# Kernel tuning notes

Hardware: AMD Instinct MI355X
Metric: run time of the kernel (lower is better)

The kernel has to match this reference:

```python
import jax, jax.numpy as jnp
import numpy as np

E = 8        # num_experts
TOPK = 2     # num_experts_per_tok
D = 1024     # n_embd
H = 2816     # grok FFN hidden dim (multiple_of-rounded 2/3*4*D)
B, T = 4, 2048
COEFF = 0.01 # moe_aux_loss_coeff


def setup_inputs() -> dict:
    key = jax.random.key(0)
    ks = jax.random.split(key, 8)
    s = 0.02  # weight scale so activations stay well-conditioned
    return {
        "x": jax.random.normal(ks[0], (B, T, D), jnp.float32),
        "gate_w": jax.random.normal(ks[1], (D, E), jnp.float32) * s,
        "expert_gate": jax.random.normal(ks[2], (E, D, H), jnp.float32) * s,
        "expert_up": jax.random.normal(ks[3], (E, D, H), jnp.float32) * s,
        "expert_down": jax.random.normal(ks[4], (E, H, D), jnp.float32) * s,
        "shared_gate": jax.random.normal(ks[5], (D, H), jnp.float32) * s,
        "shared_up": jax.random.normal(ks[6], (D, H), jnp.float32) * s,
        "shared_down": jax.random.normal(ks[7], (H, D), jnp.float32) * s,
    }


def _grok_ffn(x, g, u, d):
    # down(gelu(gate(x)) * up(x)); torch F.gelu default = exact erf gelu
    return (jax.nn.gelu(x @ g, approximate=False) * (x @ u)) @ d


def reference(x, gate_w, expert_gate, expert_up, expert_down,
              shared_gate, shared_up, shared_down):
    Bb, Tt, Dd = x.shape
    N = Bb * Tt
    xf = x.reshape(N, Dd)

    # --- router ---
    logits = (xf @ gate_w).astype(jnp.float32)            # (N, E)
    top_logits, top_idx = jax.lax.top_k(logits, TOPK)     # (N, K)
    top_w = jax.nn.softmax(top_logits, axis=-1)           # (N, K)
    gates = jax.nn.softmax(logits, axis=-1)               # (N, E)
    f = jnp.mean(jax.nn.one_hot(top_idx[:, 0], E, dtype=jnp.float32), axis=0)
    P = gates.mean(axis=0)
    aux_loss = COEFF * E * jnp.sum(f * P)

    # dense combine weights (N, E): 0 for unassigned experts
    comb = jnp.zeros((N, E), xf.dtype).at[
        jnp.arange(N)[:, None], top_idx].add(top_w.astype(xf.dtype))

    # --- experts: loop over small fixed E, weight-masked dense FFN ---
    out = jnp.zeros_like(xf)
    for e in range(E):
        ye = _grok_ffn(xf, expert_gate[e], expert_up[e], expert_down[e])
        out = out + comb[:, e:e + 1] * ye

    out = out.reshape(Bb, Tt, Dd)
    out = out + _grok_ffn(xf, shared_gate, shared_up, shared_down).reshape(Bb, Tt, Dd)
    return out, aux_loss
```

## Files before the change

kernel.cpp:

```cpp
#include <hip/hip_runtime.h>
#include <hip/hip_bf16.h>

#define NTOK 8192
#define DIM  1024
#define HID  2816
#define ROWS_CAP 25600
#define TCAP 200

typedef __bf16 bf16x8 __attribute__((ext_vector_type(8)));
typedef float  f32x4  __attribute__((ext_vector_type(4)));

__device__ __forceinline__ unsigned short f2bf(float f) {
  unsigned int x = __float_as_uint(f);
  unsigned int r = (x + 0x7fffu + ((x >> 16) & 1u)) >> 16;
  return (unsigned short)r;
}
__device__ __forceinline__ float gelu_erf(float g) {
  return 0.5f * g * (1.0f + erff(g * 0.70710678118654752f));
}

__device__ __forceinline__ void gload16(const void* g, void* l) {
  __builtin_amdgcn_global_load_lds(
      (__attribute__((address_space(1))) void*)(g),
      (__attribute__((address_space(3))) void*)(l), 16, 0, 0);
}

__device__ __forceinline__ void pipe_barrier() {
  asm volatile("s_waitcnt vmcnt(0)" ::: "memory");
  __builtin_amdgcn_s_barrier();
  __builtin_amdgcn_sched_barrier(0);
}


__global__ __launch_bounds__(256) void k_cast_bf16(const float4* __restrict__ in,
                                                   ushort4* __restrict__ out, int n4) {
  int i = blockIdx.x * 256 + threadIdx.x;
  if (i >= n4) return;
  float4 v = in[i];
  out[i] = make_ushort4(f2bf(v.x), f2bf(v.y), f2bf(v.z), f2bf(v.w));
}

__global__ __launch_bounds__(256) void k_transpose_bf16(const float* __restrict__ in,
                                                        unsigned short* __restrict__ out,
                                                        int R, int C) {
  __shared__ float t[32][33];
  size_t base = (size_t)blockIdx.z * R * C;
  in += base; out += base;
  int c0 = blockIdx.x * 32, r0 = blockIdx.y * 32;
  int tx = threadIdx.x, ty = threadIdx.y;
  #pragma unroll
  for (int i = ty; i < 32; i += 8)
    t[i][tx] = in[(size_t)(r0 + i) * C + c0 + tx];
  __syncthreads();
  #pragma unroll
  for (int i = ty; i < 32; i += 8)
    out[(size_t)(c0 + i) * R + r0 + tx] = f2bf(t[tx][i]);
}


__global__ __launch_bounds__(256) void k_router(const float* __restrict__ x,
                                                const float* __restrict__ gw,
                                                int* __restrict__ top_idx,
                                                float* __restrict__ top_w,
                                                int* __restrict__ counts,
                                                float* __restrict__ f_cnt,
                                                float* __restrict__ P_sum) {
  __shared__ float s_p[8];
  __shared__ int   s_cnt[8];
  __shared__ int   s_f[8];
  int tid = threadIdx.x;
  if (tid < 8) { s_p[tid] = 0.f; s_cnt[tid] = 0; s_f[tid] = 0; }
  __syncthreads();

  int lane = tid & 63, wv = tid >> 6;
  float ploc[8] = {0,0,0,0,0,0,0,0};
  int   cloc[8] = {0,0,0,0,0,0,0,0};
  int   floc[8] = {0,0,0,0,0,0,0,0};

  for (int t = blockIdx.x * 4 + wv; t < NTOK; t += 1024) {
    const float* xr = x + (size_t)t * DIM;
    float acc[8] = {0.f,0.f,0.f,0.f,0.f,0.f,0.f,0.f};
    for (int d = lane; d < DIM; d += 64) {
      float xv = xr[d];
      const float* g = gw + d * 8;
      #pragma unroll
      for (int e = 0; e < 8; ++e) acc[e] += xv * g[e];
    }
    #pragma unroll
    for (int e = 0; e < 8; ++e) {
      #pragma unroll
      for (int off = 32; off > 0; off >>= 1)
        acc[e] += __shfl_xor(acc[e], off, 64);
    }
    if (lane == 0) {
      int i1 = 0; float l1 = acc[0];
      #pragma unroll
      for (int e = 1; e < 8; ++e) if (acc[e] > l1) { l1 = acc[e]; i1 = e; }
      int i2 = -1; float l2 = -3.0e38f;
      #pragma unroll
      for (int e = 0; e < 8; ++e) if (e != i1 && acc[e] > l2) { l2 = acc[e]; i2 = e; }
      float e2 = expf(l2 - l1);
      float inv12 = 1.0f / (1.0f + e2);
      top_idx[2 * t] = i1; top_idx[2 * t + 1] = i2;
      top_w[2 * t] = inv12; top_w[2 * t + 1] = e2 * inv12;
      float s = 0.f, p[8];
      #pragma unroll
      for (int e = 0; e < 8; ++e) { p[e] = expf(acc[e] - l1); s += p[e]; }
      float invs = 1.0f / s;
      #pragma unroll
      for (int e = 0; e < 8; ++e) {
        ploc[e] += p[e] * invs;
        cloc[e] += (e == i1) + (e == i2);
        floc[e] += (e == i1);
      }
    }
  }
  if (lane == 0) {
    #pragma unroll
    for (int e = 0; e < 8; ++e) {
      atomicAdd(&s_p[e], ploc[e]);
      atomicAdd(&s_cnt[e], cloc[e]);
      atomicAdd(&s_f[e], floc[e]);
    }
  }
  __syncthreads();
  if (tid < 8) {
    atomicAdd(&P_sum[tid], s_p[tid]);
    atomicAdd(&counts[tid], s_cnt[tid]);
    atomicAdd(&f_cnt[tid], (float)s_f[tid]);
  }
}


__global__ __launch_bounds__(256) void k_setup(const int* __restrict__ counts,
                                               int* __restrict__ cursors,
                                               int* __restrict__ tile_expert,
                                               int* __restrict__ tile_row0,
                                               int* __restrict__ perm,
                                               float* __restrict__ wrow) {
  int t = threadIdx.x;
  for (int r = t; r < ROWS_CAP; r += 256) {
    perm[r] = (r < NTOK) ? r : 0;
    wrow[r] = (r < NTOK) ? 1.0f : 0.0f;
  }
  if (t == 0) {
    int so[8], pe[8];
    int cur = NTOK;
    for (int e = 0; e < 8; ++e) {
      so[e] = cur;
      pe[e] = ((counts[e] + 127) >> 7) << 7;
      cur += pe[e];
    }
    for (int e = 0; e < 8; ++e) cursors[e] = so[e];
    for (int tile = 0; tile < TCAP; ++tile) {
      int r0 = tile << 7;
      int ex;
      if (tile < NTOK / 128) ex = 8;
      else if (r0 < cur) {
        ex = 0;
        for (int e = 0; e < 8; ++e) if (r0 >= so[e] && r0 < so[e] + pe[e]) ex = e;
      } else ex = -1;
      tile_expert[tile] = ex;
      tile_row0[tile] = r0;
    }
  }
}

__global__ __launch_bounds__(256) void k_scatter(const int* __restrict__ top_idx,
                                                 const float* __restrict__ top_w,
                                                 int* __restrict__ cursors,
                                                 int* __restrict__ perm,
                                                 float* __restrict__ wrow) {
  int i = blockIdx.x * 256 + threadIdx.x;
  if (i < NTOK * 2) {
    int e = top_idx[i];
    float w = top_w[i];
    int slot = atomicAdd(&cursors[e], 1);
    perm[slot] = i >> 1;
    wrow[slot] = w;
  }
}


__global__ __launch_bounds__(256) void k_stageA(const unsigned short* __restrict__ xb,
    const unsigned short* __restrict__ WgT, const unsigned short* __restrict__ WuT,
    const unsigned short* __restrict__ SgT, const unsigned short* __restrict__ SuT,
    const int* __restrict__ perm,
    const int* __restrict__ tile_expert, const int* __restrict__ tile_row0,
    unsigned short* __restrict__ h, int t0, int row_base) {
  int tile = t0 + blockIdx.y;
  int e = tile_expert[tile];
  if (e < 0) return;
  const unsigned short* Bg = (e < 8) ? WgT + (size_t)e * HID * DIM : SgT;
  const unsigned short* Bu = (e < 8) ? WuT + (size_t)e * HID * DIM : SuT;
  int rows0 = tile_row0[tile];
  int h0 = blockIdx.x * 64;

  __shared__ unsigned short As[2][128 * 64];
  __shared__ unsigned short Bgs[2][64 * 64];
  __shared__ unsigned short Bus[2][64 * 64];

  int tid = threadIdx.x, lane = tid & 63, wv = tid >> 6;
  int wr = wv >> 1, wc = wv & 1;
  int rlo = lane >> 3;
  int koff = (((lane & 7) ^ rlo) * 8);
  int rsw = (lane & 7) << 4;

  const unsigned short* ap[4];
  #pragma unroll
  for (int i = 0; i < 4; ++i)
    ap[i] = xb + (size_t)perm[rows0 + i * 32 + wv * 8 + rlo] * DIM + koff;
  const unsigned short* bgp[2];
  const unsigned short* bup[2];
  #pragma unroll
  for (int i = 0; i < 2; ++i) {
    int bn = h0 + i * 32 + wv * 8 + rlo;
    bgp[i] = Bg + (size_t)bn * DIM + koff;
    bup[i] = Bu + (size_t)bn * DIM + koff;
  }

  f32x4 accg[4][2] = {};
  f32x4 accu[4][2] = {};

  auto stage = [&](int b, int k0) {
    #pragma unroll
    for (int i = 0; i < 4; ++i)
      gload16(ap[i] + k0, (char*)As[b] + (i * 32 + wv * 8) * 128);
    #pragma unroll
    for (int i = 0; i < 2; ++i) {
      gload16(bgp[i] + k0, (char*)Bgs[b] + (i * 32 + wv * 8) * 128);
      gload16(bup[i] + k0, (char*)Bus[b] + (i * 32 + wv * 8) * 128);
    }
  };

  stage(0, 0);
  pipe_barrier();
  int cur = 0;

  for (int kb = 0; kb < DIM / 64; ++kb) {
    if (kb < DIM / 64 - 1) stage(cur ^ 1, (kb + 1) * 64);
    __builtin_amdgcn_s_setprio(1);
    #pragma unroll
    for (int kk = 0; kk < 2; ++kk) {
      int kbyte = (kk * 64 + (lane >> 4) * 16) ^ rsw;
      bf16x8 a[4], bg[2], bu[2];
      #pragma unroll
      for (int mi = 0; mi < 4; ++mi)
        a[mi] = *(const bf16x8*)((const char*)As[cur] + (wr * 64 + mi * 16 + (lane & 15)) * 128 + kbyte);
      #pragma unroll
      for (int ni = 0; ni < 2; ++ni) {
        bg[ni] = *(const bf16x8*)((const char*)Bgs[cur] + (wc * 32 + ni * 16 + (lane & 15)) * 128 + kbyte);
        bu[ni] = *(const bf16x8*)((const char*)Bus[cur] + (wc * 32 + ni * 16 + (lane & 15)) * 128 + kbyte);
      }
      #pragma unroll
      for (int mi = 0; mi < 4; ++mi) {
        #pragma unroll
        for (int ni = 0; ni < 2; ++ni) {
          accg[mi][ni] = __builtin_amdgcn_mfma_f32_16x16x32_bf16(a[mi], bg[ni], accg[mi][ni], 0, 0, 0);
          accu[mi][ni] = __builtin_amdgcn_mfma_f32_16x16x32_bf16(a[mi], bu[ni], accu[mi][ni], 0, 0, 0);
        }
      }
    }
    __builtin_amdgcn_s_setprio(0);
    pipe_barrier();
    cur ^= 1;
  }

  #pragma unroll
  for (int mi = 0; mi < 4; ++mi) {
    #pragma unroll
    for (int ni = 0; ni < 2; ++ni) {
      #pragma unroll
      for (int j = 0; j < 4; ++j) {
        int rg = rows0 - row_base + wr * 64 + mi * 16 + (lane >> 4) * 4 + j;
        int cg = h0 + wc * 32 + ni * 16 + (lane & 15);
        float g = accg[mi][ni][j];
        float u = accu[mi][ni][j];
        h[(size_t)rg * HID + cg] = f2bf(gelu_erf(g) * u);
      }
    }
  }
}


template <bool STORE>
__global__ __launch_bounds__(256) void k_stageB(const unsigned short* __restrict__ h,
    const unsigned short* __restrict__ WdT, const unsigned short* __restrict__ SdT,
    const int* __restrict__ perm, const float* __restrict__ wrow,
    const int* __restrict__ tile_expert, const int* __restrict__ tile_row0,
    float* __restrict__ out, int t0, int row_base) {
  int tile = t0 + blockIdx.y;
  int e = tile_expert[tile];
  if (e < 0) return;
  const unsigned short* Bd = (e < 8) ? WdT + (size_t)e * DIM * HID : SdT;
  int rows0 = tile_row0[tile];
  int n0 = blockIdx.x * 128;

  __shared__ unsigned short As[2][128 * 64];
  __shared__ unsigned short Bs[2][128 * 64];

  int tid = threadIdx.x, lane = tid & 63, wv = tid >> 6;
  int wr = wv >> 1, wc = wv & 1;
  int rlo = lane >> 3;
  int koff = (((lane & 7) ^ rlo) * 8);
  int rsw = (lane & 7) << 4;

  const unsigned short* apt[4];
  const unsigned short* bpt[4];
  #pragma unroll
  for (int i = 0; i < 4; ++i) {
    int r = i * 32 + wv * 8 + rlo;
    apt[i] = h + (size_t)(rows0 - row_base + r) * HID + koff;
    bpt[i] = Bd + (size_t)(n0 + r) * HID + koff;
  }

  f32x4 acc[4][4] = {};

  auto stage = [&](int b, int k0) {
    #pragma unroll
    for (int i = 0; i < 4; ++i) {
      int rb = i * 32 + wv * 8;
      gload16(apt[i] + k0, (char*)As[b] + rb * 128);
      gload16(bpt[i] + k0, (char*)Bs[b] + rb * 128);
    }
  };

  stage(0, 0);
  pipe_barrier();
  int cur = 0;

  for (int kb = 0; kb < HID / 64; ++kb) {
    if (kb < HID / 64 - 1) stage(cur ^ 1, (kb + 1) * 64);
    __builtin_amdgcn_s_setprio(1);
    #pragma unroll
    for (int kk = 0; kk < 2; ++kk) {
      int kbyte = (kk * 64 + (lane >> 4) * 16) ^ rsw;
      bf16x8 a[4], b[4];
      #pragma unroll
      for (int mi = 0; mi < 4; ++mi)
        a[mi] = *(const bf16x8*)((const char*)As[cur] + (wr * 64 + mi * 16 + (lane & 15)) * 128 + kbyte);
      #pragma unroll
      for (int ni = 0; ni < 4; ++ni)
        b[ni] = *(const bf16x8*)((const char*)Bs[cur] + (wc * 64 + ni * 16 + (lane & 15)) * 128 + kbyte);
      #pragma unroll
      for (int mi = 0; mi < 4; ++mi) {
        #pragma unroll
        for (int ni = 0; ni < 4; ++ni)
          acc[mi][ni] = __builtin_amdgcn_mfma_f32_16x16x32_bf16(a[mi], b[ni], acc[mi][ni], 0, 0, 0);
      }
    }
    __builtin_amdgcn_s_setprio(0);
    pipe_barrier();
    cur ^= 1;
  }

  #pragma unroll
  for (int mi = 0; mi < 4; ++mi) {
    #pragma unroll
    for (int j = 0; j < 4; ++j) {
      int rl = wr * 64 + mi * 16 + (lane >> 4) * 4 + j;
      int token = perm[rows0 + rl];
      float w = wrow[rows0 + rl];
      #pragma unroll
      for (int ni = 0; ni < 4; ++ni) {
        int col = n0 + wc * 64 + ni * 16 + (lane & 15);
        if (STORE) out[(size_t)token * DIM + col] = w * acc[mi][ni][j];
        else atomicAdd(&out[(size_t)token * DIM + col], w * acc[mi][ni][j]);
      }
    }
  }
}


__global__ void k_aux(const float* __restrict__ f_cnt, const float* __restrict__ P_sum,
                      float* __restrict__ aux_out) {
  if (threadIdx.x == 0 && blockIdx.x == 0) {
    float a = 0.f;
    #pragma unroll
    for (int e = 0; e < 8; ++e) a += f_cnt[e] * P_sum[e];
    a *= 0.01f * 8.f / ((float)NTOK * (float)NTOK);
    aux_out[0] = a;
  }
}


extern "C" void kernel_launch(void* const* d_in, const int* in_sizes, int n_in,
                              void* d_out, int out_size, void* d_ws, size_t ws_size,
                              hipStream_t stream) {
  const float* x  = (const float*)d_in[0];
  const float* gw = (const float*)d_in[1];
  const float* eg = (const float*)d_in[2];
  const float* eu = (const float*)d_in[3];
  const float* ed = (const float*)d_in[4];
  const float* sg = (const float*)d_in[5];
  const float* su = (const float*)d_in[6];
  const float* sd = (const float*)d_in[7];
  float* out = (float*)d_out;

  char* ws = (char*)d_ws;
  size_t off = 0;
  auto take = [&](size_t sz) { size_t o = off; off += (sz + 255) & ~(size_t)255; return o; };
  const size_t OFF_XB   = take((size_t)NTOK * DIM * 2);
  const size_t OFF_WGT  = take((size_t)8 * HID * DIM * 2);
  const size_t OFF_WUT  = take((size_t)8 * HID * DIM * 2);
  const size_t OFF_WDT  = take((size_t)8 * HID * DIM * 2);
  const size_t OFF_SGT  = take((size_t)HID * DIM * 2);
  const size_t OFF_SUT  = take((size_t)HID * DIM * 2);
  const size_t OFF_SDT  = take((size_t)HID * DIM * 2);
  const size_t OFF_TI   = take((size_t)NTOK * 2 * 4);
  const size_t OFF_TW   = take((size_t)NTOK * 2 * 4);
  const size_t OFF_PERM = take((size_t)ROWS_CAP * 4);
  const size_t OFF_WROW = take((size_t)ROWS_CAP * 4);
  const size_t OFF_STATS= take(256);
  const size_t OFF_CURS = take(256);
  const size_t OFF_TE   = take(TCAP * 4);
  const size_t OFF_TR   = take(TCAP * 4);
  const size_t OFF_H    = off;

  const size_t TILE_H_BYTES = (size_t)128 * HID * 2;
  size_t avail = (ws_size > OFF_H) ? (ws_size - OFF_H) : 0;
  int G = (int)((avail / TILE_H_BYTES < (size_t)TCAP) ? (avail / TILE_H_BYTES) : (size_t)TCAP);
  if (G < 1) return;

  unsigned short* xb  = (unsigned short*)(ws + OFF_XB);
  unsigned short* WgT = (unsigned short*)(ws + OFF_WGT);
  unsigned short* WuT = (unsigned short*)(ws + OFF_WUT);
  unsigned short* WdT = (unsigned short*)(ws + OFF_WDT);
  unsigned short* SgT = (unsigned short*)(ws + OFF_SGT);
  unsigned short* SuT = (unsigned short*)(ws + OFF_SUT);
  unsigned short* SdT = (unsigned short*)(ws + OFF_SDT);
  int* top_idx        = (int*)(ws + OFF_TI);
  float* top_w        = (float*)(ws + OFF_TW);
  int* perm           = (int*)(ws + OFF_PERM);
  float* wrow         = (float*)(ws + OFF_WROW);
  int* counts         = (int*)(ws + OFF_STATS);
  float* f_cnt        = (float*)(ws + OFF_STATS + 32);
  float* P_sum        = (float*)(ws + OFF_STATS + 64);
  int* cursors        = (int*)(ws + OFF_CURS);
  int* tile_expert    = (int*)(ws + OFF_TE);
  int* tile_row0      = (int*)(ws + OFF_TR);
  unsigned short* hbuf = (unsigned short*)(ws + OFF_H);

  hipMemsetAsync(ws + OFF_STATS, 0, 256, stream);

  k_cast_bf16<<<NTOK * DIM / 4 / 256, 256, 0, stream>>>((const float4*)x, (ushort4*)xb, NTOK * DIM / 4);
  k_transpose_bf16<<<dim3(HID / 32, DIM / 32, 8), dim3(32, 8), 0, stream>>>(eg, WgT, DIM, HID);
  k_transpose_bf16<<<dim3(HID / 32, DIM / 32, 8), dim3(32, 8), 0, stream>>>(eu, WuT, DIM, HID);
  k_transpose_bf16<<<dim3(DIM / 32, HID / 32, 8), dim3(32, 8), 0, stream>>>(ed, WdT, HID, DIM);
  k_transpose_bf16<<<dim3(HID / 32, DIM / 32, 1), dim3(32, 8), 0, stream>>>(sg, SgT, DIM, HID);
  k_transpose_bf16<<<dim3(HID / 32, DIM / 32, 1), dim3(32, 8), 0, stream>>>(su, SuT, DIM, HID);
  k_transpose_bf16<<<dim3(DIM / 32, HID / 32, 1), dim3(32, 8), 0, stream>>>(sd, SdT, HID, DIM);

  k_router<<<256, 256, 0, stream>>>(x, gw, top_idx, top_w, counts, f_cnt, P_sum);
  k_setup<<<1, 256, 0, stream>>>(counts, cursors, tile_expert, tile_row0, perm, wrow);
  k_scatter<<<NTOK * 2 / 256, 256, 0, stream>>>(top_idx, top_w, cursors, perm, wrow);

  for (int t0 = 0; t0 < TCAP; t0 += G) {
    int nt = (TCAP - t0 < G) ? (TCAP - t0) : G;
    int row_base = t0 * 128;
    k_stageA<<<dim3(HID / 64, nt), 256, 0, stream>>>(xb, WgT, WuT, SgT, SuT, perm,
                                                     tile_expert, tile_row0, hbuf, t0, row_base);
    int ns = 0;
    if (t0 < 64) { ns = 64 - t0; if (ns > nt) ns = nt; }
    int ne = nt - ns;
    if (ns > 0)
      k_stageB<true><<<dim3(DIM / 128, ns), 256, 0, stream>>>(hbuf, WdT, SdT, perm, wrow,
                                                              tile_expert, tile_row0, out, t0, row_base);
    if (ne > 0)
      k_stageB<false><<<dim3(DIM / 128, ne), 256, 0, stream>>>(hbuf, WdT, SdT, perm, wrow,
                                                               tile_expert, tile_row0, out, t0 + ns, row_base);
  }

  k_aux<<<1, 64, 0, stream>>>(f_cnt, P_sum, out + (size_t)NTOK * DIM);
}
```

Baseline: 1.072 ms.

## Load A operand directly from global into registers, bypassing LDS staging

In both GEMM stages the activation (A) tile is no longer staged through double-buffered shared memory. Each wave instead loads its own MFMA A fragments straight from global memory into registers at the start of each k-block. This removes the A LDS traffic and footprint, which may raise occupancy. The cost is synchronous global loads with no prefetch, and A rows are re-read by both column-waves (wc), so A traffic to L2 doubles and load latency is exposed.

```diff
diff --git a/kernel.cpp b/kernel.cpp
--- a/kernel.cpp
+++ b/kernel.cpp
@@ -196,7 +196,6 @@
   int rows0 = tile_row0[tile];
   int h0 = blockIdx.x * 64;
 
-  __shared__ unsigned short As[2][128 * 64];
   __shared__ unsigned short Bgs[2][64 * 64];
   __shared__ unsigned short Bus[2][64 * 64];
 
@@ -208,8 +207,9 @@
 
   const unsigned short* ap[4];
   #pragma unroll
-  for (int i = 0; i < 4; ++i)
-    ap[i] = xb + (size_t)perm[rows0 + i * 32 + wv * 8 + rlo] * DIM + koff;
+  for (int mi = 0; mi < 4; ++mi)
+    ap[mi] = xb + (size_t)perm[rows0 + wr * 64 + mi * 16 + (lane & 15)] * DIM + (lane >> 4) * 8;
+
   const unsigned short* bgp[2];
   const unsigned short* bup[2];
   #pragma unroll
@@ -224,9 +224,6 @@
 
   auto stage = [&](int b, int k0) {
     #pragma unroll
-    for (int i = 0; i < 4; ++i)
-      gload16(ap[i] + k0, (char*)As[b] + (i * 32 + wv * 8) * 128);
-    #pragma unroll
     for (int i = 0; i < 2; ++i) {
       gload16(bgp[i] + k0, (char*)Bgs[b] + (i * 32 + wv * 8) * 128);
       gload16(bup[i] + k0, (char*)Bus[b] + (i * 32 + wv * 8) * 128);
@@ -239,14 +236,18 @@
 
   for (int kb = 0; kb < DIM / 64; ++kb) {
     if (kb < DIM / 64 - 1) stage(cur ^ 1, (kb + 1) * 64);
+    bf16x8 a[4][2];
+    #pragma unroll
+    for (int mi = 0; mi < 4; ++mi) {
+      #pragma unroll
+      for (int kk = 0; kk < 2; ++kk)
+        a[mi][kk] = *(const bf16x8*)(ap[mi] + kb * 64 + kk * 32);
+    }
     __builtin_amdgcn_s_setprio(1);
     #pragma unroll
     for (int kk = 0; kk < 2; ++kk) {
       int kbyte = (kk * 64 + (lane >> 4) * 16) ^ rsw;
-      bf16x8 a[4], bg[2], bu[2];
-      #pragma unroll
-      for (int mi = 0; mi < 4; ++mi)
-        a[mi] = *(const bf16x8*)((const char*)As[cur] + (wr * 64 + mi * 16 + (lane & 15)) * 128 + kbyte);
+      bf16x8 bg[2], bu[2];
       #pragma unroll
       for (int ni = 0; ni < 2; ++ni) {
         bg[ni] = *(const bf16x8*)((const char*)Bgs[cur] + (wc * 32 + ni * 16 + (lane & 15)) * 128 + kbyte);
@@ -256,8 +257,8 @@
       for (int mi = 0; mi < 4; ++mi) {
         #pragma unroll
         for (int ni = 0; ni < 2; ++ni) {
-          accg[mi][ni] = __builtin_amdgcn_mfma_f32_16x16x32_bf16(a[mi], bg[ni], accg[mi][ni], 0, 0, 0);
-          accu[mi][ni] = __builtin_amdgcn_mfma_f32_16x16x32_bf16(a[mi], bu[ni], accu[mi][ni], 0, 0, 0);
+          accg[mi][ni] = __builtin_amdgcn_mfma_f32_16x16x32_bf16(a[mi][kk], bg[ni], accg[mi][ni], 0, 0, 0);
+          accu[mi][ni] = __builtin_amdgcn_mfma_f32_16x16x32_bf16(a[mi][kk], bu[ni], accu[mi][ni], 0, 0, 0);
         }
       }
     }
@@ -296,7 +297,6 @@
   int rows0 = tile_row0[tile];
   int n0 = blockIdx.x * 128;
 
-  __shared__ unsigned short As[2][128 * 64];
   __shared__ unsigned short Bs[2][128 * 64];
 
   int tid = threadIdx.x, lane = tid & 63, wv = tid >> 6;
@@ -305,12 +305,15 @@
   int koff = (((lane & 7) ^ rlo) * 8);
   int rsw = (lane & 7) << 4;
 
-  const unsigned short* apt[4];
+  const unsigned short* ap[4];
+  #pragma unroll
+  for (int mi = 0; mi < 4; ++mi)
+    ap[mi] = h + (size_t)(rows0 - row_base + wr * 64 + mi * 16 + (lane & 15)) * HID + (lane >> 4) * 8;
+
   const unsigned short* bpt[4];
   #pragma unroll
   for (int i = 0; i < 4; ++i) {
     int r = i * 32 + wv * 8 + rlo;
-    apt[i] = h + (size_t)(rows0 - row_base + r) * HID + koff;
     bpt[i] = Bd + (size_t)(n0 + r) * HID + koff;
   }
 
@@ -318,11 +321,8 @@
 
   auto stage = [&](int b, int k0) {
     #pragma unroll
-    for (int i = 0; i < 4; ++i) {
-      int rb = i * 32 + wv * 8;
-      gload16(apt[i] + k0, (char*)As[b] + rb * 128);
-      gload16(bpt[i] + k0, (char*)Bs[b] + rb * 128);
-    }
+    for (int i = 0; i < 4; ++i)
+      gload16(bpt[i] + k0, (char*)Bs[b] + (i * 32 + wv * 8) * 128);
   };
 
   stage(0, 0);
@@ -331,14 +331,18 @@
 
   for (int kb = 0; kb < HID / 64; ++kb) {
     if (kb < HID / 64 - 1) stage(cur ^ 1, (kb + 1) * 64);
+    bf16x8 a[4][2];
+    #pragma unroll
+    for (int mi = 0; mi < 4; ++mi) {
+      #pragma unroll
+      for (int kk = 0; kk < 2; ++kk)
+        a[mi][kk] = *(const bf16x8*)(ap[mi] + kb * 64 + kk * 32);
+    }
     __builtin_amdgcn_s_setprio(1);
     #pragma unroll
     for (int kk = 0; kk < 2; ++kk) {
       int kbyte = (kk * 64 + (lane >> 4) * 16) ^ rsw;
-      bf16x8 a[4], b[4];
-      #pragma unroll
-      for (int mi = 0; mi < 4; ++mi)
-        a[mi] = *(const bf16x8*)((const char*)As[cur] + (wr * 64 + mi * 16 + (lane & 15)) * 128 + kbyte);
+      bf16x8 b[4];
       #pragma unroll
       for (int ni = 0; ni < 4; ++ni)
         b[ni] = *(const bf16x8*)((const char*)Bs[cur] + (wc * 64 + ni * 16 + (lane & 15)) * 128 + kbyte);
@@ -346,7 +350,7 @@
       for (int mi = 0; mi < 4; ++mi) {
         #pragma unroll
         for (int ni = 0; ni < 4; ++ni)
-          acc[mi][ni] = __builtin_amdgcn_mfma_f32_16x16x32_bf16(a[mi], b[ni], acc[mi][ni], 0, 0, 0);
+          acc[mi][ni] = __builtin_amdgcn_mfma_f32_16x16x32_bf16(a[mi][kk], b[ni], acc[mi][ni], 0, 0, 0);
       }
     }
     __builtin_amdgcn_s_setprio(0);
```

Result: slower. 1.369 ms (+27.6%).
